# Optimization experiments

Measured on AMD Instinct MI355X. Metric: run time of the kernel, lower is better.

## Reference

```python
import jax, jax.numpy as jnp
import numpy as np

K = 3          # patch_size
PAD = 1        # (K-1)//2
EPS = 1e-8
STYLE_STRENGTH = 1.0


def _whiten(x):
    # WCT whitening: zero-mean, multiply by Cov^{-1/2} (eigendecomposition)
    B, C, H, W = x.shape
    f = x.reshape(B, C, H * W)
    f = f - f.mean(-1, keepdims=True)
    cov = jnp.einsum('bcn,bdn->bcd', f, f) / (H * W - 1)
    e, v = jnp.linalg.eigh(cov)
    d = 1.0 / jnp.sqrt(jnp.maximum(e, EPS))
    wmat = jnp.einsum('bce,be,bde->bcd', v, d, v)   # V diag(e^-1/2) V^T
    return jnp.einsum('bcd,bdn->bcn', wmat, f).reshape(B, C, H, W)


def _color(x, target):
    # WCT coloring: multiply by style Cov^{1/2}, add style mean
    B, C, H, W = x.shape
    f = x.reshape(B, C, H * W)
    t = target.reshape(B, C, -1)
    tm = t.mean(-1, keepdims=True)
    tc = t - tm
    cov = jnp.einsum('bcn,bdn->bcd', tc, tc) / (tc.shape[-1] - 1)
    e, v = jnp.linalg.eigh(cov)
    d = jnp.sqrt(jnp.maximum(e, 0.0))
    cmat = jnp.einsum('bce,be,bde->bcd', v, d, v)   # V diag(e^1/2) V^T
    out = jnp.einsum('bcd,bdn->bcn', cmat, f) + tm
    return out.reshape(B, C, H, W)


def _extract_patches(x):
    # [B,C,H,W] -> [B,H*W,C,K*K], zero padding, stride 1 (matches torch unfold order)
    B, C, H, W = x.shape
    xp = jnp.pad(x, ((0, 0), (0, 0), (PAD, PAD), (PAD, PAD)))
    pats = jnp.stack([xp[:, :, i:i + H, j:j + W] for i in range(K) for j in range(K)], axis=-1)
    return pats.reshape(B, C, H * W, K * K).transpose(0, 2, 1, 3)


def _style_decorator(content_feature, style_feature):
    nc = _whiten(content_feature)
    ns = _whiten(style_feature)
    B, C, H, W = nc.shape
    P = ns.shape[2] * ns.shape[3]                     # number of style patches
    kern = _extract_patches(ns).reshape(B, P, C * K * K)
    knorm = jnp.linalg.norm(kern, axis=2, keepdims=True) + 1e-5
    cpat = _extract_patches(nc).reshape(B, H * W, C * K * K)
    # conv2d with normalized style kernels == cosine-similarity cross-correlation
    score = jnp.einsum('bqm,bpm->bpq', cpat, kern / knorm)    # [B, P, H*W]
    # binarization_patch_score: per-pixel argmax over style patches (one-hot),
    # then deconv with UNNORMALIZED kernels == gather the winning kernel per pixel
    idx = jnp.argmax(score, axis=1)                           # [B, H*W]
    gathered = jnp.take_along_axis(kern, idx[:, :, None], axis=1)  # [B, H*W, C*K*K]
    G = gathered.reshape(B, H, W, C, K, K).transpose(0, 3, 1, 2, 4, 5)  # [B,C,H,W,K,K]
    # conv_transpose2d(pad=K-1) on zero-padded one-hot == overlap-add of kernels
    full = jnp.zeros((B, C, H + K - 1, W + K - 1), dtype=nc.dtype)
    for dx in range(K):
        for dy in range(K):
            full = full.at[:, :, dx:dx + H, dy:dy + W].add(G[..., dx, dy])
    out = full[:, :, PAD:PAD + H, PAD:PAD + W]
    # norm_deconvolution: overlap counts (static)
    nfull = np.zeros((H + K - 1, W + K - 1), dtype=np.float32)
    for dx in range(K):
        for dy in range(K):
            nfull[dx:dx + H, dy:dy + W] += 1.0
    dn = jnp.asarray(nfull[PAD:PAD + H, PAD:PAD + W])
    reassembled = out / dn
    stylized = _color(reassembled, style_feature)
    return (1.0 - STYLE_STRENGTH) * content_feature + STYLE_STRENGTH * stylized


def setup_inputs() -> dict:
    key = jax.random.key(0)
    k1, k2 = jax.random.split(key)
    return {
        'content_feature': jax.random.normal(k1, (2, 512, 64, 64), dtype=jnp.float32),
        'style_feature': jax.random.normal(k2, (2, 512, 64, 64), dtype=jnp.float32),
    }


def reference(content_feature, style_feature):
    return _style_decorator(content_feature, style_feature)
```

## Files before the change

kernel.cpp:

```cpp
#include <hip/hip_runtime.h>


#define CH    512
#define NPIX  4096
#define HPAD  66
#define PPAD  4356
#define MROWS 4480
#define S0W   4480
#define NS_ITERS 7

typedef unsigned short u16;
typedef _Float16 half8 __attribute__((ext_vector_type(8)));
typedef __attribute__((ext_vector_type(4))) float f32x4;

__device__ __forceinline__ float f16tof(u16 h){
  union { u16 u; _Float16 f; } v; v.u = h; return (float)v.f;
}
__device__ __forceinline__ void split2(float x, u16& h, u16& l){
  _Float16 hf = (_Float16)x;
  float r = (x - (float)hf) * 2048.0f;
  union { u16 u; _Float16 f; } hv, lv;
  hv.f = hf; lv.f = (_Float16)r;
  h = hv.u; l = lv.u;
}
__device__ __forceinline__ void gll16(const void* g, void* l){
  __builtin_amdgcn_global_load_lds((const __attribute__((address_space(1))) unsigned*)g,
                                   (__attribute__((address_space(3))) unsigned*)l,
                                   16, 0, 0);
}
__device__ __forceinline__ f32x4 mfma_f16(half8 a, half8 b, f32x4 c){
  return __builtin_amdgcn_mfma_f32_16x16x32_f16(a, b, c, 0, 0, 0);
}

enum { M_COVP = 0, M_NST = 1, M_X3 = 2, M_WHITEN = 3, M_S0 = 4, M_COLOR = 5 };

struct GP {
  const u16 *Ah, *Al, *Bh, *Bl;
  const u16 *Eh, *El, *Fh, *Fl;
  size_t sAz, sBz;
  float* Cf;
  u16 *Ch, *Cl;
  u16 *Gh, *Gl;
  size_t sCz;
  const float* scales;
  const float* meanv;
  int K;
  int Kit;
};

template<int TILE, int MODE, int KSTEP = 32>
__global__ __launch_bounds__(256, 2)
void gemm_sp(GP p){
  constexpr int MF = TILE / 32;
  constexpr int SLOTS = KSTEP / 8;
  constexpr int TSUB = KSTEP / 32;
  constexpr bool SYM = (MODE == M_NST) || (MODE == M_X3);
  int z = blockIdx.z;
  int m0, n0;
  int kbase = 0;
  int za = z, zout = z;
  bool mirror = false;
  if constexpr (MODE == M_COVP){
    const int b = blockIdx.x;
    const int xcd = b & 7, w = b >> 3;
    const int zc = xcd*2 + (w & 1);
    const int tile = w >> 1;
    m0 = (tile >> 3)*64; n0 = (tile & 7)*64;
    kbase = (zc & 3) * p.Kit;
    za = zc >> 2; zout = zc;
  } else if constexpr (SYM){
    int bx = blockIdx.x;
    int ty = 0;
    while((ty+1)*(ty+2)/2 <= bx) ++ty;
    int tx = bx - ty*(ty+1)/2;
    m0 = ty*64; n0 = tx*64; mirror = (tx != ty);
  } else if constexpr (MODE == M_S0){
    const int b = blockIdx.x;
    const int x = b & 7;
    int rem = b >> 3;
    int g = 0, R = 0, mo = 0;
    for(; g < 5; ++g){
      mo = (x + 3*g) & 7;
      R = (mo < 3) ? 5 : 4;
      if(rem < R*7) break;
      rem -= R*7;
    }
    if(g == 5) return;
    const int mi = rem / 7, ni = rem % 7;
    m0 = (mo + mi*8) * 128;
    n0 = (g*7 + ni) * 128;
  } else if constexpr (MODE == M_WHITEN){
    const int b = blockIdx.x;
    const int x = b & 7, w = b >> 3;
    z = x >> 1;
    const int mt = (x & 1) + (w >> 2) * 2;
    m0 = mt * 128;
    n0 = (w & 3) * 128;
    za = z; zout = z;
  } else {
    m0 = blockIdx.y*TILE; n0 = blockIdx.x*TILE;
  }

  const u16 *Ah, *Al, *Bh, *Bl;
  if constexpr (MODE == M_X3){
    const size_t zb = (size_t)(z & 3) * CH * CH;
    if(z < 4){ Ah=p.Ah+zb; Al=p.Al+zb; Bh=p.Bh+zb; Bl=p.Bl+zb; }
    else     { Ah=p.Eh+zb; Al=p.El+zb; Bh=p.Fh+zb; Bl=p.Fl+zb; }
  } else {
    Ah = p.Ah + (size_t)za * p.sAz;
    Al = p.Al + (size_t)za * p.sAz;
    Bh = p.Bh + (size_t)za * p.sBz;
    Bl = p.Bl + (size_t)za * p.sBz;
  }

  const int tid = threadIdx.x, ln = tid & 63, wv = tid >> 6;
  const int wm = (wv >> 1) * (TILE/2), wn = (wv & 1) * (TILE/2);
  __shared__ __align__(16) u16 sAh[2][TILE*KSTEP], sAl[2][TILE*KSTEP];
  __shared__ __align__(16) u16 sBh[2][TILE*KSTEP], sBl[2][TILE*KSTEP];
  f32x4 acc1[MF][MF], acc2[MF][MF];
#pragma unroll
  for(int i=0;i<MF;++i)
#pragma unroll
    for(int j=0;j<MF;++j){ acc1[i][j] = (f32x4)0.0f; acc2[i][j] = (f32x4)0.0f; }
  const int K = p.K;

  auto stage = [&](int k0, int buf){
#pragma unroll
    for(int s = tid; s < TILE*SLOTS; s += 256){
      const int row = s / SLOTS, pos = s % SLOTS;
      const int kc = pos ^ ((row >> 2) & (SLOTS-1));
      const size_t ga = (size_t)(m0 + row) * K + k0 + kc*8;
      const size_t gb = (size_t)(n0 + row) * K + k0 + kc*8;
      gll16(Ah + ga, sAh[buf] + s*8);
      gll16(Al + ga, sAl[buf] + s*8);
      gll16(Bh + gb, sBh[buf] + s*8);
      gll16(Bl + gb, sBl[buf] + s*8);
    }
  };

  stage(kbase, 0);
  int cur = 0;
  for(int kk = 0; kk < p.Kit; kk += KSTEP){
    __syncthreads();
    if(kk + KSTEP < p.Kit) stage(kbase + kk + KSTEP, cur ^ 1);
    const u16* pAh = sAh[cur]; const u16* pAl = sAl[cur];
    const u16* pBh = sBh[cur]; const u16* pBl = sBl[cur];
#pragma unroll
    for(int t = 0; t < TSUB; ++t){
      half8 ah[MF], al[MF], bh[MF], bl[MF];
#pragma unroll
      for(int i=0;i<MF;++i){
        const int ra = wm + i*16 + (ln & 15);
        const int rb = wn + i*16 + (ln & 15);
        const int pa = (t*4 + (ln >> 4)) ^ ((ra >> 2) & (SLOTS-1));
        const int pb = (t*4 + (ln >> 4)) ^ ((rb >> 2) & (SLOTS-1));
        const int ofa = ra*KSTEP + pa*8;
        const int ofb = rb*KSTEP + pb*8;
        ah[i] = *(const half8*)(pAh + ofa);
        al[i] = *(const half8*)(pAl + ofa);
        bh[i] = *(const half8*)(pBh + ofb);
        bl[i] = *(const half8*)(pBl + ofb);
      }
#pragma unroll
      for(int i=0;i<MF;++i)
#pragma unroll
        for(int j=0;j<MF;++j){
          acc1[i][j] = mfma_f16(ah[i], bh[j], acc1[i][j]);
          acc2[i][j] = mfma_f16(ah[i], bl[j], acc2[i][j]);
          acc2[i][j] = mfma_f16(al[i], bh[j], acc2[i][j]);
        }
    }
    cur ^= 1;
  }
  u16 *C0 = nullptr, *C1 = nullptr;
  if constexpr (MODE == M_NST){
    const size_t zb = (size_t)z * p.sCz;
    C0 = p.Ch + zb; C1 = p.Cl + zb;
  } else if constexpr (MODE == M_X3){
    const size_t zb = (size_t)(z & 3) * p.sCz;
    if(z < 4){ C0 = p.Ch + zb; C1 = p.Cl + zb; }
    else     { C0 = p.Gh + zb; C1 = p.Gl + zb; }
  }
#pragma unroll
  for(int i=0;i<MF;++i)
#pragma unroll
    for(int j=0;j<MF;++j)
#pragma unroll
      for(int r=0;r<4;++r){
        const int m = m0 + wm + i*16 + (ln >> 4)*4 + r;
        const int n = n0 + wn + j*16 + (ln & 15);
        float v = acc1[i][j][r] + acc2[i][j][r] * (1.0f/2048.0f);
        if constexpr (MODE == M_COVP){
          p.Cf[(size_t)zout * p.sCz + (size_t)m * CH + n] = v;
        } else if constexpr (MODE == M_NST || MODE == M_X3){
          if constexpr (MODE == M_NST) v = -0.5f*v + ((m == n) ? 1.5f : 0.0f);
          u16 h, l; split2(v, h, l);
          C0[(size_t)m*CH + n] = h; C1[(size_t)m*CH + n] = l;
          if(mirror){
            C0[(size_t)n*CH + m] = h; C1[(size_t)n*CH + m] = l;
          }
        } else if constexpr (MODE == M_WHITEN){
          v *= p.scales[z*4 + 3];
          const int prow = ((m >> 6) + 1)*HPAD + (m & 63) + 1;
          u16 h, l; split2(v, h, l);
          const size_t o = (size_t)z*p.sCz + (size_t)prow*CH + n;
          p.Ch[o] = h; p.Cl[o] = l;
        } else if constexpr (MODE == M_S0){
          p.Cf[(size_t)m * S0W + n] = v;
        } else {
          const float sc = p.scales[(2+z)*4 + 2];
          const float mu = p.meanv[(2+z)*CH + m];
          p.Cf[(size_t)z*p.sCz + (size_t)m*NPIX + n] = v*sc + mu;
        }
      }
}

__global__ __launch_bounds__(256)
void cov_reduce_kernel(const float* __restrict__ covp, float* __restrict__ cov,
                       float* __restrict__ rowsum){
  size_t t = (size_t)blockIdx.x * 256 + threadIdx.x;
  int z = (int)(t >> 18);
  size_t e = t & 262143;
  float s = 0.f;
#pragma unroll
  for(int c = 0; c < 4; ++c) s += covp[((size_t)(z*4 + c) << 18) + e];
  s *= (1.0f / 4095.0f);
  cov[t] = s;
  __shared__ float red[256];
  red[threadIdx.x] = fabsf(s); __syncthreads();
  for(int w = 128; w > 0; w >>= 1){
    if(threadIdx.x < w) red[threadIdx.x] += red[threadIdx.x + w];
    __syncthreads();
  }
  if(threadIdx.x == 0){
    int row = (int)(e >> 9);
    atomicAdd(&rowsum[z*512 + row], red[0]);
  }
}

__global__ __launch_bounds__(256)
void scale_fin_kernel(const float* __restrict__ rowsum, float* __restrict__ scales){
  __shared__ float red[256];
  for(int z = 0; z < 4; ++z){
    float m = fmaxf(rowsum[z*512 + threadIdx.x], rowsum[z*512 + 256 + threadIdx.x]);
    red[threadIdx.x] = m; __syncthreads();
    for(int w = 128; w > 0; w >>= 1){
      if(threadIdx.x < w) red[threadIdx.x] = fmaxf(red[threadIdx.x], red[threadIdx.x + w]);
      __syncthreads();
    }
    if(threadIdx.x == 0){
      float c = red[0];
      scales[z*4+0] = c;
      scales[z*4+1] = 1.0f / c;
      scales[z*4+2] = sqrtf(c);
      scales[z*4+3] = rsqrtf(c);
    }
    __syncthreads();
  }
}

__global__ __launch_bounds__(256)
void mean_kernel(const float* __restrict__ content, const float* __restrict__ style,
                 float* __restrict__ meanv){
  int mm = blockIdx.x;
  int z = mm >> 9, c = mm & 511;
  const float* X = ((z < 2) ? content + (size_t)z * CH * NPIX
                            : style   + (size_t)(z - 2) * CH * NPIX) + (size_t)c * NPIX;
  float s = 0.f;
  for(int i = threadIdx.x; i < NPIX; i += 256) s += X[i];
  __shared__ float red[256];
  red[threadIdx.x] = s; __syncthreads();
  for(int w = 128; w > 0; w >>= 1){
    if(threadIdx.x < w) red[threadIdx.x] += red[threadIdx.x + w];
    __syncthreads();
  }
  if(threadIdx.x == 0) meanv[mm] = red[0] * (1.0f / NPIX);
}

__global__ __launch_bounds__(256)
void center_split_kernel(const float* __restrict__ content, const float* __restrict__ style,
                         const float* __restrict__ meanv,
                         u16* __restrict__ Xch, u16* __restrict__ Xcl,
                         u16* __restrict__ XcTh, u16* __restrict__ XcTl){
  int z = blockIdx.z;
  const float* X = (z < 2) ? content + (size_t)z * CH * NPIX
                           : style   + (size_t)(z - 2) * CH * NPIX;
  int p0 = blockIdx.x * 64, c0 = blockIdx.y * 64;
  __shared__ float T[64][65];
  int col = threadIdx.x & 63, rq = threadIdx.x >> 6;
#pragma unroll
  for(int i = 0; i < 16; ++i){
    int r = i*4 + rq;
    int c = c0 + r;
    float v = X[(size_t)c * NPIX + p0 + col] - meanv[z*CH + c];
    u16 h, l; split2(v, h, l);
    size_t o = (size_t)(z*CH + c) * NPIX + p0 + col;
    Xch[o] = h; Xcl[o] = l;
    T[col][r] = v;
  }
  __syncthreads();
#pragma unroll
  for(int i = 0; i < 16; ++i){
    int r = i*4 + rq;
    float v = T[r][col];
    u16 h, l; split2(v, h, l);
    size_t o = (size_t)(z*NPIX + p0 + r) * CH + c0 + col;
    XcTh[o] = h; XcTl[o] = l;
  }
}

__global__ __launch_bounds__(256)
void ns_init_kernel(const float* __restrict__ cov, const float* __restrict__ scales,
                    u16* Yh, u16* Yl, u16* Zh, u16* Zl){
  size_t t = (size_t)blockIdx.x * 256 + threadIdx.x;
  int z = (int)(t >> 18);
  size_t e = t & 262143;
  int row = (int)(e >> 9), col = (int)(e & 511);
  float v = cov[t] * scales[z*4+1];
  u16 h, l; split2(v, h, l);
  Yh[t] = h; Yl[t] = l;
  Zh[t] = (row == col) ? (u16)0x3C00 : (u16)0;
  Zl[t] = 0;
}

__global__ __launch_bounds__(256)
void cn2_kernel(const u16* __restrict__ Wh, const u16* __restrict__ Wl,
                float* __restrict__ cn2){
  int b = blockIdx.y;
  int row = blockIdx.x * 16 + (threadIdx.x >> 4);
  int t = threadIdx.x & 15;
  float s = 0.f;
  if(row < PPAD){
    size_t base = ((size_t)(2 + b) * MROWS + row) * CH;
    for(int ch = t; ch < 64; ch += 16){
      uint4 hv = *(const uint4*)(Wh + base + ch*8);
      uint4 lv = *(const uint4*)(Wl + base + ch*8);
      const unsigned* hw = (const unsigned*)&hv;
      const unsigned* lw = (const unsigned*)&lv;
#pragma unroll
      for(int w = 0; w < 4; ++w){
        float v0 = f16tof((u16)(hw[w] & 0xFFFF)) + f16tof((u16)(lw[w] & 0xFFFF))*(1.0f/2048.0f);
        float v1 = f16tof((u16)(hw[w] >> 16))    + f16tof((u16)(lw[w] >> 16))*(1.0f/2048.0f);
        s = fmaf(v0, v0, s); s = fmaf(v1, v1, s);
      }
    }
  }
  for(int off = 8; off; off >>= 1) s += __shfl_down(s, off, 16);
  if(t == 0 && row < PPAD) cn2[b*PPAD + row] = s;
}

__global__ __launch_bounds__(256)
void rnorm_kernel(const float* __restrict__ cn2, float* __restrict__ rnorm){
  int b = blockIdx.y;
  int p = blockIdx.x * 256 + threadIdx.x;
  int py = p >> 6, px = p & 63;
  const float* c2 = cn2 + (size_t)b * PPAD + (size_t)py * HPAD + px;
  float s = 0.f;
#pragma unroll
  for(int i = 0; i < 3; ++i)
#pragma unroll
    for(int j = 0; j < 3; ++j) s += c2[i * HPAD + j];
  rnorm[b * 4096 + p] = 1.0f / (sqrtf(s) + 1e-5f);
}

__device__ __forceinline__ unsigned long long score_key(float s, int p){
  unsigned u = __float_as_uint(s);
  u = (u & 0x80000000u) ? ~u : (u | 0x80000000u);
  return ((unsigned long long)u << 32) | (unsigned long long)(0xFFFFFFFFu - (unsigned)p);
}

__global__ __launch_bounds__(256)
void score_partial_kernel(const float* __restrict__ S0T, const float* __restrict__ rnorm,
                          unsigned long long* __restrict__ skey, int b){
  const int blk = blockIdx.x;
  const int xcd = blk & 7, w = blk >> 3;
  const int chunk = xcd*8 + (w & 7);
  const int qg = w >> 3;
  const int t = threadIdx.x;
  const int q0 = qg*512 + t, q1 = q0 + 256;
  const int qc0 = (q0 >> 6)*HPAD + (q0 & 63);
  const int qc1 = (q1 >> 6)*HPAD + (q1 & 63);
  const float* rn = rnorm + b * 4096;
  float b0 = -1e30f, b1 = -1e30f; int i0 = 0, i1 = 0;
  for(int p = chunk*64; p < chunk*64 + 64; ++p){
    const size_t base = (size_t)((p >> 6)*HPAD + (p & 63)) * S0W;
    float s0 = 0.f, s1 = 0.f;
#pragma unroll
    for(int i = 0; i < 3; ++i)
#pragma unroll
      for(int j = 0; j < 3; ++j){
        const size_t d = (size_t)(i*HPAD + j) * (S0W + 1);
        s0 += S0T[base + qc0 + d];
        s1 += S0T[base + qc1 + d];
      }
    const float r = rn[p];
    s0 *= r; s1 *= r;
    if(s0 > b0){ b0 = s0; i0 = p; }
    if(s1 > b1){ b1 = s1; i1 = p; }
  }
  atomicMax(skey + (size_t)b*4096 + q0, score_key(b0, i0));
  atomicMax(skey + (size_t)b*4096 + q1, score_key(b1, i1));
}

__global__ __launch_bounds__(256)
void gather_kernel(const u16* __restrict__ Wh, const u16* __restrict__ Wl,
                   const unsigned long long* __restrict__ skey,
                   u16* __restrict__ RTh, u16* __restrict__ RTl){
  int g = blockIdx.x * 256 + threadIdx.x;
  int cg = g & 63;
  int pix = (g >> 6) & 4095;
  int b = g >> 18;
  int y = pix >> 6, x = pix & 63;
  const unsigned long long* kb = skey + (size_t)b * 4096;
  size_t matbase = (size_t)(2 + b) * MROWS * CH;
  float a8[8] = {0,0,0,0,0,0,0,0};
  int cnt = 0;
#pragma unroll
  for(int i = 0; i < 3; ++i){
    int qy = y + 1 - i;
    if((unsigned)qy >= 64u) continue;
#pragma unroll
    for(int j = 0; j < 3; ++j){
      int qx = x + 1 - j;
      if((unsigned)qx >= 64u) continue;
      int p = (int)(0xFFFFFFFFu - (unsigned)(kb[qy * 64 + qx] & 0xFFFFFFFFull));
      int row = ((p >> 6) + i) * HPAD + (p & 63) + j;
      size_t off = matbase + (size_t)row * CH + cg * 8;
      uint4 hv = *(const uint4*)(Wh + off);
      uint4 lv = *(const uint4*)(Wl + off);
      const unsigned* hw = (const unsigned*)&hv;
      const unsigned* lw = (const unsigned*)&lv;
#pragma unroll
      for(int w = 0; w < 4; ++w){
        a8[2*w]   += f16tof((u16)(hw[w] & 0xFFFF)) + f16tof((u16)(lw[w] & 0xFFFF))*(1.0f/2048.0f);
        a8[2*w+1] += f16tof((u16)(hw[w] >> 16))    + f16tof((u16)(lw[w] >> 16))*(1.0f/2048.0f);
      }
      ++cnt;
    }
  }
  float inv = 1.0f / (float)cnt;
  u16 oh[8], ol[8];
#pragma unroll
  for(int k = 0; k < 8; ++k){
    float v = a8[k] * inv;
    split2(v, oh[k], ol[k]);
  }
  size_t ro = ((size_t)(b * 4096 + pix)) * CH + cg * 8;
  *(uint4*)(RTh + ro) = *(const uint4*)oh;
  *(uint4*)(RTl + ro) = *(const uint4*)ol;
}

extern "C" void kernel_launch(void* const* d_in, const int* in_sizes, int n_in,
                              void* d_out, int out_size, void* d_ws, size_t ws_size,
                              hipStream_t stream){
  (void)in_sizes; (void)n_in; (void)out_size; (void)ws_size;
  const float* content = (const float*)d_in[0];
  const float* style   = (const float*)d_in[1];
  float* out = (float*)d_out;

  char* base = (char*)d_ws;
  size_t off = 0;
  auto take = [&](size_t nbytes) -> char* {
    char* p = base + off;
    off = (off + nbytes + 255) & ~(size_t)255;
    return p;
  };
  const size_t MAT = (size_t)CH*CH*2;
  const size_t FEAT = (size_t)CH*NPIX*2;
  const size_t WMAT = (size_t)MROWS*CH*2;
  const size_t S0SZ = (size_t)MROWS*S0W*4;

  float* meanv  = (float*)take((size_t)4*CH*sizeof(float));
  float* scales = (float*)take(256);
  float* rowsum = (float*)take((size_t)4*CH*sizeof(float));
  float* cov    = (float*)take((size_t)4*CH*CH*sizeof(float));
  u16 *Yh=(u16*)take(4*MAT), *Yl=(u16*)take(4*MAT);
  u16 *Zh=(u16*)take(4*MAT), *Zl=(u16*)take(4*MAT);
  u16 *Th=(u16*)take(4*MAT), *Tl=(u16*)take(4*MAT);
  u16 *Ynh=(u16*)take(4*MAT), *Ynl=(u16*)take(4*MAT);
  u16 *Znh=(u16*)take(4*MAT), *Znl=(u16*)take(4*MAT);
  float* covp = (float*)Yh;
  char* P1 = take(2*(size_t)4*WMAT);
  u16 *Xch=(u16*)P1, *Xcl=(u16*)(P1+4*FEAT);
  u16 *Wh=(u16*)P1,  *Wl=(u16*)(P1+4*WMAT);
  char* P0 = take(S0SZ);
  u16 *XcTh=(u16*)P0, *XcTl=(u16*)(P0+4*FEAT);
  float* S0T = (float*)P0;
  u16 *RTh=(u16*)P0, *RTl=(u16*)(P0+2*FEAT);
  float* cn2    = (float*)take((size_t)2*PPAD*sizeof(float));
  float* rnormb = (float*)take((size_t)2*4096*sizeof(float));
  unsigned long long* skey = (unsigned long long*)take((size_t)2*4096*8);

  hipMemsetAsync(rowsum, 0, (size_t)4*CH*sizeof(float), stream);
  hipMemsetAsync(skey, 0, (size_t)2*4096*8, stream);

  mean_kernel<<<2048, 256, 0, stream>>>(content, style, meanv);
  center_split_kernel<<<dim3(64, 8, 4), 256, 0, stream>>>(content, style, meanv,
                                                          Xch, Xcl, XcTh, XcTl);
  {
    GP g{}; g.Ah=Xch; g.Al=Xcl; g.Bh=Xch; g.Bl=Xcl;
    g.sAz = g.sBz = (size_t)CH*NPIX; g.Cf = covp; g.sCz = (size_t)CH*CH;
    g.K = NPIX; g.Kit = 1024;
    gemm_sp<64, M_COVP, 32><<<dim3(1024), 256, 0, stream>>>(g);
  }
  cov_reduce_kernel<<<4096, 256, 0, stream>>>(covp, cov, rowsum);
  scale_fin_kernel<<<1, 256, 0, stream>>>(rowsum, scales);
  ns_init_kernel<<<4096, 256, 0, stream>>>(cov, scales, Yh, Yl, Zh, Zl);

  u16 *Ach[2]={Yh,Yl}, *Bch[2]={Zh,Zl}, *An[2]={Ynh,Ynl}, *Bn[2]={Znh,Znl};
  for(int it = 0; it < NS_ITERS; ++it){
    GP t{}; t.Ah=Bch[0]; t.Al=Bch[1];
    t.Bh=Ach[0]; t.Bl=Ach[1];
    t.sAz = t.sBz = (size_t)CH*CH; t.Ch=Th; t.Cl=Tl; t.sCz=(size_t)CH*CH;
    t.K = CH; t.Kit = CH;
    gemm_sp<64, M_NST, 64><<<dim3(36, 1, 4), 256, 0, stream>>>(t);
    GP u{}; u.Ah=Ach[0]; u.Al=Ach[1];
    u.Bh=Th; u.Bl=Tl;
    u.Eh=Th; u.El=Tl;
    u.Fh=Bch[0]; u.Fl=Bch[1];
    u.Ch=An[0]; u.Cl=An[1];
    u.Gh=Bn[0]; u.Gl=Bn[1];
    u.sCz=(size_t)CH*CH; u.K = CH; u.Kit = CH;
    gemm_sp<64, M_X3, 64><<<dim3(36, 1, 8), 256, 0, stream>>>(u);
    for(int c = 0; c < 2; ++c){ u16* tmp=Ach[c]; Ach[c]=An[c]; An[c]=tmp;
                                tmp=Bch[c]; Bch[c]=Bn[c]; Bn[c]=tmp; }
  }

  hipMemsetAsync(Wh, 0, 4*WMAT, stream);
  hipMemsetAsync(Wl, 0, 4*WMAT, stream);
  {
    GP w{}; w.Ah=XcTh; w.Al=XcTl; w.sAz=(size_t)NPIX*CH;
    w.Bh=Bch[0]; w.Bl=Bch[1]; w.sBz=(size_t)CH*CH;
    w.Ch=Wh; w.Cl=Wl; w.sCz=(size_t)MROWS*CH; w.scales=scales;
    w.K = CH; w.Kit = CH;
    gemm_sp<128, M_WHITEN, 32><<<dim3(512), 256, 0, stream>>>(w);
  }
  cn2_kernel<<<dim3(273, 2), 256, 0, stream>>>(Wh, Wl, cn2);
  rnorm_kernel<<<dim3(16, 2), 256, 0, stream>>>(cn2, rnormb);

  for(int b = 0; b < 2; ++b){
    GP s{};
    s.Ah = Wh + (size_t)(2+b)*MROWS*CH; s.Al = Wl + (size_t)(2+b)*MROWS*CH;
    s.Bh = Wh + (size_t)b*MROWS*CH;     s.Bl = Wl + (size_t)b*MROWS*CH;
    s.sAz = s.sBz = 0; s.Cf = S0T; s.sCz = 0; s.K = CH; s.Kit = CH;
    gemm_sp<128, M_S0, 32><<<dim3(1232), 256, 0, stream>>>(s);
    score_partial_kernel<<<dim3(512), 256, 0, stream>>>(S0T, rnormb, skey, b);
  }

  gather_kernel<<<2048, 256, 0, stream>>>(Wh, Wl, skey, RTh, RTl);
  {
    GP c{}; c.Ah = Ach[0] + 2*(size_t)CH*CH; c.Al = Ach[1] + 2*(size_t)CH*CH;
    c.sAz = (size_t)CH*CH;
    c.Bh = RTh; c.Bl = RTl; c.sBz = (size_t)NPIX*CH;
    c.Cf = out; c.sCz = (size_t)CH*NPIX; c.scales = scales; c.meanv = meanv;
    c.K = CH; c.Kit = CH;
    gemm_sp<128, M_COLOR, 32><<<dim3(32, 4, 2), 256, 0, stream>>>(c);
  }
}
```

Measured before the change: 725.4 us.

## Use single-buffered LDS with higher occupancy for large-tile GEMMs

Adds template options to the split-precision GEMM that select single or double LDS buffering and set the launch-bounds occupancy. The 128-tile whiten, score and color GEMMs now use a single buffer with two barriers per k-step and target 4 blocks per CU. This halves shared memory per block so more blocks can hide latency through occupancy instead of software prefetch. The cost is losing the overlap of global loads with MFMA inside a block, and a tighter register budget that may cause spills with 4x4 fragment accumulators.

```diff
diff --git a/kernel.cpp b/kernel.cpp
--- a/kernel.cpp
+++ b/kernel.cpp
@@ -48,12 +48,13 @@
   int Kit;
 };
 
-template<int TILE, int MODE, int KSTEP = 32>
-__global__ __launch_bounds__(256, 2)
+template<int TILE, int MODE, int KSTEP = 32, bool DBUF = true, int OCC = 2>
+__global__ __launch_bounds__(256, OCC)
 void gemm_sp(GP p){
   constexpr int MF = TILE / 32;
   constexpr int SLOTS = KSTEP / 8;
   constexpr int TSUB = KSTEP / 32;
+  constexpr int NBUF = DBUF ? 2 : 1;
   constexpr bool SYM = (MODE == M_NST) || (MODE == M_X3);
   int z = blockIdx.z;
   int m0, n0;
@@ -115,8 +116,8 @@
 
   const int tid = threadIdx.x, ln = tid & 63, wv = tid >> 6;
   const int wm = (wv >> 1) * (TILE/2), wn = (wv & 1) * (TILE/2);
-  __shared__ __align__(16) u16 sAh[2][TILE*KSTEP], sAl[2][TILE*KSTEP];
-  __shared__ __align__(16) u16 sBh[2][TILE*KSTEP], sBl[2][TILE*KSTEP];
+  __shared__ __align__(16) u16 sAh[NBUF][TILE*KSTEP], sAl[NBUF][TILE*KSTEP];
+  __shared__ __align__(16) u16 sBh[NBUF][TILE*KSTEP], sBl[NBUF][TILE*KSTEP];
   f32x4 acc1[MF][MF], acc2[MF][MF];
 #pragma unroll
   for(int i=0;i<MF;++i)
@@ -138,13 +139,9 @@
     }
   };
 
-  stage(kbase, 0);
-  int cur = 0;
-  for(int kk = 0; kk < p.Kit; kk += KSTEP){
-    __syncthreads();
-    if(kk + KSTEP < p.Kit) stage(kbase + kk + KSTEP, cur ^ 1);
-    const u16* pAh = sAh[cur]; const u16* pAl = sAl[cur];
-    const u16* pBh = sBh[cur]; const u16* pBl = sBl[cur];
+  auto compute = [&](int buf){
+    const u16* pAh = sAh[buf]; const u16* pAl = sAl[buf];
+    const u16* pBh = sBh[buf]; const u16* pBl = sBl[buf];
 #pragma unroll
     for(int t = 0; t < TSUB; ++t){
       half8 ah[MF], al[MF], bh[MF], bl[MF];
@@ -170,7 +167,24 @@
           acc2[i][j] = mfma_f16(al[i], bh[j], acc2[i][j]);
         }
     }
-    cur ^= 1;
+  };
+
+  if constexpr (DBUF){
+    stage(kbase, 0);
+    int cur = 0;
+    for(int kk = 0; kk < p.Kit; kk += KSTEP){
+      __syncthreads();
+      if(kk + KSTEP < p.Kit) stage(kbase + kk + KSTEP, cur ^ 1);
+      compute(cur);
+      cur ^= 1;
+    }
+  } else {
+    for(int kk = 0; kk < p.Kit; kk += KSTEP){
+      stage(kbase + kk, 0);
+      __syncthreads();
+      compute(0);
+      __syncthreads();
+    }
   }
   u16 *C0 = nullptr, *C1 = nullptr;
   if constexpr (MODE == M_NST){
@@ -533,7 +547,7 @@
     w.Bh=Bch[0]; w.Bl=Bch[1]; w.sBz=(size_t)CH*CH;
     w.Ch=Wh; w.Cl=Wl; w.sCz=(size_t)MROWS*CH; w.scales=scales;
     w.K = CH; w.Kit = CH;
-    gemm_sp<128, M_WHITEN, 32><<<dim3(512), 256, 0, stream>>>(w);
+    gemm_sp<128, M_WHITEN, 32, false, 4><<<dim3(512), 256, 0, stream>>>(w);
   }
   cn2_kernel<<<dim3(273, 2), 256, 0, stream>>>(Wh, Wl, cn2);
   rnorm_kernel<<<dim3(16, 2), 256, 0, stream>>>(cn2, rnormb);
@@ -543,7 +557,7 @@
     s.Ah = Wh + (size_t)(2+b)*MROWS*CH; s.Al = Wl + (size_t)(2+b)*MROWS*CH;
     s.Bh = Wh + (size_t)b*MROWS*CH;     s.Bl = Wl + (size_t)b*MROWS*CH;
     s.sAz = s.sBz = 0; s.Cf = S0T; s.sCz = 0; s.K = CH; s.Kit = CH;
-    gemm_sp<128, M_S0, 32><<<dim3(1232), 256, 0, stream>>>(s);
+    gemm_sp<128, M_S0, 32, false, 4><<<dim3(1232), 256, 0, stream>>>(s);
     score_partial_kernel<<<dim3(512), 256, 0, stream>>>(S0T, rnormb, skey, b);
   }
 
@@ -554,6 +568,6 @@
     c.Bh = RTh; c.Bl = RTl; c.sBz = (size_t)NPIX*CH;
     c.Cf = out; c.sCz = (size_t)CH*NPIX; c.scales = scales; c.meanv = meanv;
     c.K = CH; c.Kit = CH;
-    gemm_sp<128, M_COLOR, 32><<<dim3(32, 4, 2), 256, 0, stream>>>(c);
-  }
-}
+    gemm_sp<128, M_COLOR, 32, false, 4><<<dim3(32, 4, 2), 256, 0, stream>>>(c);
+  }
+}
```

Result: slower. 1.803 ms (+148.6%).
